# Kernel optimization log

Hardware: AMD Instinct MI355X
Metric: run time of the kernel (lower is better)

Reference implementation:

```python
import jax, jax.numpy as jnp
import numpy as np

B, S, D, H, DK, CR = 4, 4096, 1024, 16, 64, 3


def setup_inputs() -> dict:
    rng = jax.random.key(0)
    ks = jax.random.split(rng, 13)
    sc = 1.0 / np.sqrt(D)
    u = lambda k, shape: jax.random.uniform(k, shape, jnp.float32, -sc, sc)
    return {
        "query": jax.random.normal(ks[0], (B, S, D), jnp.float32),
        "key": jax.random.normal(ks[1], (B, S, D), jnp.float32),
        "value": jax.random.normal(ks[2], (B, S, D), jnp.float32),
        "Wq": u(ks[3], (D, D)), "bq": u(ks[4], (D,)),
        "Wk": u(ks[5], (D, D)), "bk": u(ks[6], (D,)),
        "Wv": u(ks[7], (D, D)), "bv": u(ks[8], (D,)),
        "Wo": u(ks[9], (D, D)), "bo": u(ks[10], (D,)),
        "conv_w": u(ks[11], (D, D, CR)),  # Conv1d(D, D, kernel=CR, stride=CR)
        "conv_b": u(ks[12], (D,)),
    }


def _compress(x, w, b):
    # x: (B, L, D) -> strided conv over L -> (B, ceil-ish L/CR, D)
    y = jax.lax.conv_general_dilated(
        x.transpose(0, 2, 1), w, window_strides=(CR,), padding="VALID",
        dimension_numbers=("NCH", "OIH", "NCH"))
    return (y + b[None, :, None]).transpose(0, 2, 1)


def reference(query, key, value, Wq, bq, Wk, bk, Wv, bv, Wo, bo, conv_w, conv_b):
    # Source quirk: pad amount derived from d_model (last dim), applied to seq.
    pad = CR - D % CR  # = 2 here
    if pad < CR:
        key = jnp.pad(key, ((0, 0), (pad, 0), (0, 0)))
        value = jnp.pad(value, ((0, 0), (pad, 0), (0, 0)))
    key = _compress(key, conv_w, conv_b)
    value = _compress(value, conv_w, conv_b)

    def proj(x, W, bias):  # (B, L, D) -> (B, H, L, DK)
        return (x @ W.T + bias).reshape(x.shape[0], -1, H, DK).transpose(0, 2, 1, 3)

    q = proj(query, Wq, bq)
    k = proj(key, Wk, bk)
    v = proj(value, Wv, bv)

    scores = jnp.einsum("bhqd,bhkd->bhqk", q, k) / np.float32(np.sqrt(DK))
    attn = jax.nn.softmax(scores, axis=-1)  # dropout is identity at eval
    x = jnp.einsum("bhqk,bhkd->bhqd", attn, v)
    x = x.transpose(0, 2, 1, 3).reshape(query.shape[0], -1, H * DK)
    return x @ Wo.T + bo
```

## Files before the change

### kernel.cpp

```cpp
#include <hip/hip_runtime.h>


#define DM   1024
#define NH   16
#define DKH  64
#define BB   4
#define SQ   4096
#define LCC  1366
#define LCP  1408
#define SPAD 4098
#define PSS  72

#define QSC  0.18033688011f

typedef unsigned short u16;
using short8 = __attribute__((ext_vector_type(8))) short;
using f32x4  = __attribute__((ext_vector_type(4))) float;
using us4    = __attribute__((ext_vector_type(4))) unsigned short;
using us8    = __attribute__((ext_vector_type(8))) unsigned short;

__device__ __forceinline__ u16 f2bf(float f) {
    unsigned u = __float_as_uint(f);
    u += 0x7fffu + ((u >> 16) & 1u);
    return (u16)(u >> 16);
}

__device__ __forceinline__ void gl_lds16(const void* g, void* l) {
    __builtin_amdgcn_global_load_lds(
        (__attribute__((address_space(1))) unsigned int*)(uintptr_t)g,
        (__attribute__((address_space(3))) unsigned int*)l,
        16, 0, 0);
}

__global__ __launch_bounds__(256) void cast4_k(const float* __restrict__ in, u16* __restrict__ out,
                                               int n4, float scale) {
    int i = blockIdx.x * 256 + threadIdx.x;
    if (i >= n4) return;
    float4 v = ((const float4*)in)[i];
    us4 o;
    o[0] = f2bf(v.x * scale); o[1] = f2bf(v.y * scale);
    o[2] = f2bf(v.z * scale); o[3] = f2bf(v.w * scale);
    ((us4*)out)[i] = o;
}

__global__ __launch_bounds__(256) void cast_pad_k(const float* __restrict__ in, u16* __restrict__ out) {
    int i = blockIdx.x * 256 + threadIdx.x;
    const int n4 = BB * SPAD * DM / 4;
    if (i >= n4) return;
    int e   = i * 4;
    int b   = e / (SPAD * DM);
    int rem = e - b * (SPAD * DM);
    int s   = rem >> 10;
    int d   = rem & (DM - 1);
    us4 o = {0, 0, 0, 0};
    if (s >= 2) {
        float4 v = *(const float4*)(in + (size_t)(b * SQ + (s - 2)) * DM + d);
        o[0] = f2bf(v.x); o[1] = f2bf(v.y); o[2] = f2bf(v.z); o[3] = f2bf(v.w);
    }
    ((us4*)out)[i] = o;
}

__global__ __launch_bounds__(256) void permcast_conv_k(const float* __restrict__ cw, u16* __restrict__ wc2) {
    int i = blockIdx.x * 256 + threadIdx.x;
    const int n4 = DM * DM * 3 / 4;
    if (i >= n4) return;
    int e   = i * 4;
    int o   = e / 3072;
    int rem = e - o * 3072;
    int r   = rem >> 10;
    int ii  = rem & 1023;
    us4 q;
    #pragma unroll
    for (int t = 0; t < 4; ++t) q[t] = f2bf(cw[(size_t)(o * DM + ii + t) * 3 + r]);
    ((us4*)wc2)[i] = q;
}

__global__ __launch_bounds__(256) void transpose_v_k(const u16* __restrict__ vp, u16* __restrict__ vt) {
    __shared__ u16 t[64 * 65];
    const int tid = threadIdx.x;
    const int j0 = blockIdx.x * 64;
    const int bh = blockIdx.y, b = bh >> 4, h = bh & 15;
    #pragma unroll
    for (int it = 0; it < 2; ++it) {
        int cc = tid + it * 256;
        int j = cc >> 3, d0 = (cc & 7) * 8;
        int jj = j0 + j;
        us8 v = {0, 0, 0, 0, 0, 0, 0, 0};
        if (jj < LCC) v = *(const us8*)(vp + (size_t)(b * LCC + jj) * DM + h * DKH + d0);
        #pragma unroll
        for (int q = 0; q < 8; ++q) t[(d0 + q) * 65 + j] = v[q];
    }
    __syncthreads();
    #pragma unroll
    for (int it = 0; it < 2; ++it) {
        int cc = tid + it * 256;
        int d = cc >> 3, q0 = (cc & 7) * 8;
        us8 v;
        #pragma unroll
        for (int q = 0; q < 8; ++q) {
            int cp = q0 + q;
            int k  = (cp & 3) * 16 + (cp >> 2);
            v[q] = t[d * 65 + k];
        }
        *(us8*)(vt + (size_t)(bh * DKH + d) * LCP + j0 + q0) = v;
    }
}

__global__ __launch_bounds__(256, 3) void gemm_mfma_k(
    const u16* __restrict__ A, const u16* __restrict__ Bw, const float* __restrict__ bias,
    void* __restrict__ C, int N, int K, int cf32, float bscale)
{
    __shared__ u16 As[128 * 64];
    __shared__ u16 Bs[128 * 64];
    const int tid = threadIdx.x, wave = tid >> 6, lane = tid & 63;
    const int quad = lane >> 4, l15 = lane & 15;
    const int n0 = blockIdx.y * 128, o0 = blockIdx.x * 128;
    const int wm = (wave >> 1) * 64, wn = (wave & 1) * 64;

    f32x4 acc[4][4];
    #pragma unroll
    for (int a = 0; a < 4; ++a)
        #pragma unroll
        for (int b = 0; b < 4; ++b)
            #pragma unroll
            for (int r = 0; r < 4; ++r) acc[a][b][r] = 0.0f;

    const int srow = (lane >> 3);
    const int sc8  = (lane & 7);

    for (int kt = 0; kt < K; kt += 64) {
        #pragma unroll
        for (int i = 0; i < 4; ++i) {
            int is  = wave * 4 + i;
            int row = is * 8 + srow;
            int c   = sc8 ^ (row & 7);
            int ra  = n0 + row; if (ra > N - 1) ra = N - 1;
            gl_lds16(A  + (size_t)ra * K + kt + c * 8,          As + is * 512 + lane * 8);
            gl_lds16(Bw + (size_t)(o0 + row) * K + kt + c * 8,  Bs + is * 512 + lane * 8);
        }
        __syncthreads();
        #pragma unroll
        for (int ks = 0; ks < 2; ++ks) {
            short8 af[4], bf[4];
            #pragma unroll
            for (int mi = 0; mi < 4; ++mi) {
                int m = wm + mi * 16 + l15;
                int c = (ks * 4 + quad) ^ (m & 7);
                af[mi] = *(const short8*)(As + m * 64 + c * 8);
            }
            #pragma unroll
            for (int nj = 0; nj < 4; ++nj) {
                int n = wn + nj * 16 + l15;
                int c = (ks * 4 + quad) ^ (n & 7);
                bf[nj] = *(const short8*)(Bs + n * 64 + c * 8);
            }
            #pragma unroll
            for (int mi = 0; mi < 4; ++mi)
                #pragma unroll
                for (int nj = 0; nj < 4; ++nj)
                    acc[mi][nj] = __builtin_amdgcn_mfma_f32_16x16x32_bf16(af[mi], bf[nj], acc[mi][nj], 0, 0, 0);
        }
        __syncthreads();
    }
    #pragma unroll
    for (int mi = 0; mi < 4; ++mi) {
        #pragma unroll
        for (int r = 0; r < 4; ++r) {
            int n = n0 + wm + mi * 16 + quad * 4 + r;
            if (n < N) {
                #pragma unroll
                for (int nj = 0; nj < 4; ++nj) {
                    int o = o0 + wn + nj * 16 + l15;
                    float v = acc[mi][nj][r] + bias[o] * bscale;
                    if (cf32) ((float*)C)[(size_t)n * DM + o] = v;
                    else      ((u16*)C)[(size_t)n * DM + o] = f2bf(v);
                }
            }
        }
    }
}

__global__ __launch_bounds__(256, 3) void attn_mfma_k(
    const u16* __restrict__ qp, const u16* __restrict__ kp,
    const u16* __restrict__ vt, u16* __restrict__ xo)
{
    __shared__ u16 Qs[128 * 64];
    __shared__ u16 Ks[64 * 64];
    __shared__ u16 Vts[64 * 64];
    __shared__ u16 Ps[128 * PSS];
    const int tid = threadIdx.x, wave = tid >> 6, lane = tid & 63;
    const int quad = lane >> 4, l15 = lane & 15;
    const int bh = blockIdx.y, b = bh >> 4, h = bh & 15;
    const int s0 = blockIdx.x * 128;
    const int wm = wave * 32;
    const int srow = (lane >> 3), sc8 = (lane & 7);

    #pragma unroll
    for (int i = 0; i < 4; ++i) {
        int is = wave * 4 + i;
        int row = is * 8 + srow;
        int c = sc8 ^ (row & 7);
        gl_lds16(qp + (size_t)(b * SQ + s0 + row) * DM + h * DKH + c * 8, Qs + is * 512 + lane * 8);
    }

    f32x4 oacc[2][4];
    #pragma unroll
    for (int a = 0; a < 2; ++a)
        #pragma unroll
        for (int d = 0; d < 4; ++d)
            #pragma unroll
            for (int r = 0; r < 4; ++r) oacc[a][d][r] = 0.0f;
    float lsum[2][4] = {{0.f, 0.f, 0.f, 0.f}, {0.f, 0.f, 0.f, 0.f}};

    for (int j0 = 0; j0 < LCC; j0 += 64) {
        #pragma unroll
        for (int i = 0; i < 2; ++i) {
            int is = wave * 2 + i;
            int row = is * 8 + srow;
            int c = sc8 ^ (row & 7);
            int j = j0 + row; if (j > LCC - 1) j = LCC - 1;
            gl_lds16(kp + (size_t)(b * LCC + j) * DM + h * DKH + c * 8, Ks + is * 512 + lane * 8);
            gl_lds16(vt + (size_t)(bh * DKH + row) * LCP + j0 + c * 8,  Vts + is * 512 + lane * 8);
        }
        __syncthreads();

        f32x4 sc[2][4];
        #pragma unroll
        for (int a = 0; a < 2; ++a)
            #pragma unroll
            for (int n = 0; n < 4; ++n)
                #pragma unroll
                for (int r = 0; r < 4; ++r) sc[a][n][r] = 0.0f;
        #pragma unroll
        for (int ks = 0; ks < 2; ++ks) {
            short8 aq[2], bk[4];
            #pragma unroll
            for (int mi = 0; mi < 2; ++mi) {
                int m = wm + mi * 16 + l15;
                int c = (ks * 4 + quad) ^ (m & 7);
                aq[mi] = *(const short8*)(Qs + m * 64 + c * 8);
            }
            #pragma unroll
            for (int nj = 0; nj < 4; ++nj) {
                int n = nj * 16 + l15;
                int c = (ks * 4 + quad) ^ (n & 7);
                bk[nj] = *(const short8*)(Ks + n * 64 + c * 8);
            }
            #pragma unroll
            for (int mi = 0; mi < 2; ++mi)
                #pragma unroll
                for (int nj = 0; nj < 4; ++nj)
                    sc[mi][nj] = __builtin_amdgcn_mfma_f32_16x16x32_bf16(aq[mi], bk[nj], sc[mi][nj], 0, 0, 0);
        }
        if (j0 + 64 > LCC) {
            #pragma unroll
            for (int nj = 0; nj < 4; ++nj) {
                if (j0 + nj * 16 + l15 >= LCC) {
                    #pragma unroll
                    for (int mi = 0; mi < 2; ++mi)
                        #pragma unroll
                        for (int r = 0; r < 4; ++r) sc[mi][nj][r] = -1e30f;
                }
            }
        }
        #pragma unroll
        for (int mi = 0; mi < 2; ++mi) {
            int pmb = wm + mi * 16 + quad * 4;
            #pragma unroll
            for (int r = 0; r < 4; ++r) {
                float p0 = __builtin_amdgcn_exp2f(sc[mi][0][r]);
                float p1 = __builtin_amdgcn_exp2f(sc[mi][1][r]);
                float p2 = __builtin_amdgcn_exp2f(sc[mi][2][r]);
                float p3 = __builtin_amdgcn_exp2f(sc[mi][3][r]);
                lsum[mi][r] += (p0 + p1) + (p2 + p3);
                unsigned w0, w1;
                asm("v_cvt_pk_bf16_f32 %0, %1, %2" : "=v"(w0) : "v"(p0), "v"(p1));
                asm("v_cvt_pk_bf16_f32 %0, %1, %2" : "=v"(w1) : "v"(p2), "v"(p3));
                uint2 pk; pk.x = w0; pk.y = w1;
                *(uint2*)(Ps + (pmb + r) * PSS + l15 * 4) = pk;
            }
        }
        #pragma unroll
        for (int ks = 0; ks < 2; ++ks) {
            short8 ap[2], bv[4];
            #pragma unroll
            for (int mi = 0; mi < 2; ++mi) {
                int m = wm + mi * 16 + l15;
                ap[mi] = *(const short8*)(Ps + m * PSS + ks * 32 + quad * 8);
            }
            #pragma unroll
            for (int dj = 0; dj < 4; ++dj) {
                int d = dj * 16 + l15;
                int c = (ks * 4 + quad) ^ (d & 7);
                bv[dj] = *(const short8*)(Vts + d * 64 + c * 8);
            }
            #pragma unroll
            for (int mi = 0; mi < 2; ++mi)
                #pragma unroll
                for (int dj = 0; dj < 4; ++dj)
                    oacc[mi][dj] = __builtin_amdgcn_mfma_f32_16x16x32_bf16(ap[mi], bv[dj], oacc[mi][dj], 0, 0, 0);
        }
        __syncthreads();
    }
    #pragma unroll
    for (int mi = 0; mi < 2; ++mi) {
        #pragma unroll
        for (int r = 0; r < 4; ++r) {
            float v = lsum[mi][r];
            v += __shfl_xor(v, 1, 64); v += __shfl_xor(v, 2, 64);
            v += __shfl_xor(v, 4, 64); v += __shfl_xor(v, 8, 64);
            float inv = 1.0f / v;
            int s = s0 + wm + mi * 16 + quad * 4 + r;
            #pragma unroll
            for (int dj = 0; dj < 4; ++dj)
                xo[(size_t)(b * SQ + s) * DM + h * DKH + dj * 16 + l15] = f2bf(oacc[mi][dj][r] * inv);
        }
    }
}

extern "C" void kernel_launch(void* const* d_in, const int* in_sizes, int n_in,
                              void* d_out, int out_size, void* d_ws, size_t ws_size,
                              hipStream_t stream)
{
    const float* query  = (const float*)d_in[0];
    const float* key    = (const float*)d_in[1];
    const float* value  = (const float*)d_in[2];
    const float* Wq     = (const float*)d_in[3];
    const float* bq     = (const float*)d_in[4];
    const float* Wk     = (const float*)d_in[5];
    const float* bk     = (const float*)d_in[6];
    const float* Wv     = (const float*)d_in[7];
    const float* bv     = (const float*)d_in[8];
    const float* Wo     = (const float*)d_in[9];
    const float* bo     = (const float*)d_in[10];
    const float* conv_w = (const float*)d_in[11];
    const float* conv_b = (const float*)d_in[12];
    float* out = (float*)d_out;

    u16* p = (u16*)d_ws;
    auto alloc = [&](size_t n) { u16* r = p; p += (n + 127) & ~(size_t)127; return r; };
    u16* qbf  = alloc((size_t)BB * SQ * DM);
    u16* kpad = alloc((size_t)BB * SPAD * DM);
    u16* vpad = alloc((size_t)BB * SPAD * DM);
    u16* wqb  = alloc((size_t)DM * DM);
    u16* wkb  = alloc((size_t)DM * DM);
    u16* wvb  = alloc((size_t)DM * DM);
    u16* wob  = alloc((size_t)DM * DM);
    u16* wc2b = alloc((size_t)DM * DM * 3);
    u16* kc   = alloc((size_t)BB * LCC * DM);
    u16* vc   = alloc((size_t)BB * LCC * DM);
    u16* kpj  = alloc((size_t)BB * LCC * DM);
    u16* vpj  = alloc((size_t)BB * LCC * DM);
    u16* qprj = alloc((size_t)BB * SQ * DM);
    u16* vtb  = alloc((size_t)BB * NH * DKH * LCP);
    u16* xo   = alloc((size_t)BB * SQ * DM);

    const int NC = BB * LCC;
    const int NS = BB * SQ;

    cast4_k<<<dim3(NS * DM / 4 / 256), 256, 0, stream>>>(query, qbf, NS * DM / 4, 1.0f);
    cast_pad_k<<<dim3((BB * SPAD * DM / 4 + 255) / 256), 256, 0, stream>>>(key, kpad);
    cast_pad_k<<<dim3((BB * SPAD * DM / 4 + 255) / 256), 256, 0, stream>>>(value, vpad);
    cast4_k<<<dim3(DM * DM / 4 / 256), 256, 0, stream>>>(Wq, wqb, DM * DM / 4, QSC);
    cast4_k<<<dim3(DM * DM / 4 / 256), 256, 0, stream>>>(Wk, wkb, DM * DM / 4, 1.0f);
    cast4_k<<<dim3(DM * DM / 4 / 256), 256, 0, stream>>>(Wv, wvb, DM * DM / 4, 1.0f);
    cast4_k<<<dim3(DM * DM / 4 / 256), 256, 0, stream>>>(Wo, wob, DM * DM / 4, 1.0f);
    permcast_conv_k<<<dim3(DM * DM * 3 / 4 / 256), 256, 0, stream>>>(conv_w, wc2b);

    gemm_mfma_k<<<dim3(8, 43), 256, 0, stream>>>(kpad, wc2b, conv_b, kc, NC, 3072, 0, 1.0f);
    gemm_mfma_k<<<dim3(8, 43), 256, 0, stream>>>(vpad, wc2b, conv_b, vc, NC, 3072, 0, 1.0f);

    gemm_mfma_k<<<dim3(8, 128), 256, 0, stream>>>(qbf, wqb, bq, qprj, NS, DM, 0, QSC);
    gemm_mfma_k<<<dim3(8, 43), 256, 0, stream>>>(kc, wkb, bk, kpj, NC, DM, 0, 1.0f);
    gemm_mfma_k<<<dim3(8, 43), 256, 0, stream>>>(vc, wvb, bv, vpj, NC, DM, 0, 1.0f);

    transpose_v_k<<<dim3(22, BB * NH), 256, 0, stream>>>(vpj, vtb);

    attn_mfma_k<<<dim3(SQ / 128, BB * NH), 256, 0, stream>>>(qprj, kpj, vtb, xo);

    gemm_mfma_k<<<dim3(8, 128), 256, 0, stream>>>(xo, wob, bo, out, NS, DM, 1, 1.0f);
}
```

Baseline: 670.5 us.

## Double-buffer K/V in attention, keep P in registers, batch paired launches

```diff
diff --git a/kernel.cpp b/kernel.cpp
--- a/kernel.cpp
+++ b/kernel.cpp
@@ -9,7 +9,6 @@
 #define LCC  1366
 #define LCP  1408
 #define SPAD 4098
-#define PSS  72
 
 #define QSC  0.18033688011f
 
@@ -43,7 +42,10 @@
     ((us4*)out)[i] = o;
 }
 
-__global__ __launch_bounds__(256) void cast_pad_k(const float* __restrict__ in, u16* __restrict__ out) {
+__global__ __launch_bounds__(256) void cast_pad2_k(const float* __restrict__ in0, u16* __restrict__ out0,
+                                                   const float* __restrict__ in1, u16* __restrict__ out1) {
+    const float* in = blockIdx.z ? in1 : in0;
+    u16* out        = blockIdx.z ? out1 : out0;
     int i = blockIdx.x * 256 + threadIdx.x;
     const int n4 = BB * SPAD * DM / 4;
     if (i >= n4) return;
@@ -99,7 +101,8 @@
         #pragma unroll
         for (int q = 0; q < 8; ++q) {
             int cp = q0 + q;
-            int k  = (cp & 3) * 16 + (cp >> 2);
+            int ks = cp >> 5, qd = (cp >> 3) & 3, j = cp & 7;
+            int k  = (ks + 2 * (j >> 2)) * 16 + qd * 4 + (j & 3);
             v[q] = t[d * 65 + k];
         }
         *(us8*)(vt + (size_t)(bh * DKH + d) * LCP + j0 + q0) = v;
@@ -107,9 +110,15 @@
 }
 
 __global__ __launch_bounds__(256, 3) void gemm_mfma_k(
-    const u16* __restrict__ A, const u16* __restrict__ Bw, const float* __restrict__ bias,
-    void* __restrict__ C, int N, int K, int cf32, float bscale)
+    const u16* __restrict__ A0, const u16* __restrict__ B0, const float* __restrict__ bias0, void* __restrict__ C0,
+    const u16* __restrict__ A1, const u16* __restrict__ B1, const float* __restrict__ bias1, void* __restrict__ C1,
+    int N, int K, int cf32, float bscale)
 {
+    const u16* A     = blockIdx.z ? A1 : A0;
+    const u16* Bw    = blockIdx.z ? B1 : B0;
+    const float* bias = blockIdx.z ? bias1 : bias0;
+    void* C          = blockIdx.z ? C1 : C0;
+
     __shared__ u16 As[128 * 64];
     __shared__ u16 Bs[128 * 64];
     const int tid = threadIdx.x, wave = tid >> 6, lane = tid & 63;
@@ -184,24 +193,34 @@
     const u16* __restrict__ qp, const u16* __restrict__ kp,
     const u16* __restrict__ vt, u16* __restrict__ xo)
 {
-    __shared__ u16 Qs[128 * 64];
-    __shared__ u16 Ks[64 * 64];
-    __shared__ u16 Vts[64 * 64];
-    __shared__ u16 Ps[128 * PSS];
+    __shared__ u16 lds[4 * 4096];
     const int tid = threadIdx.x, wave = tid >> 6, lane = tid & 63;
     const int quad = lane >> 4, l15 = lane & 15;
     const int bh = blockIdx.y, b = bh >> 4, h = bh & 15;
     const int s0 = blockIdx.x * 128;
-    const int wm = wave * 32;
-    const int srow = (lane >> 3), sc8 = (lane & 7);
+    const int wq = wave * 32;
+    const int srow = lane >> 3, sc8 = lane & 7;
 
     #pragma unroll
     for (int i = 0; i < 4; ++i) {
         int is = wave * 4 + i;
         int row = is * 8 + srow;
         int c = sc8 ^ (row & 7);
-        gl_lds16(qp + (size_t)(b * SQ + s0 + row) * DM + h * DKH + c * 8, Qs + is * 512 + lane * 8);
-    }
+        gl_lds16(qp + (size_t)(b * SQ + s0 + row) * DM + h * DKH + c * 8,
+                 lds + is * 512 + lane * 8);
+    }
+    __syncthreads();
+    short8 qfr[2][2];
+    #pragma unroll
+    for (int qg = 0; qg < 2; ++qg) {
+        int m = wq + qg * 16 + l15;
+        #pragma unroll
+        for (int ks = 0; ks < 2; ++ks) {
+            int c = (ks * 4 + quad) ^ (m & 7);
+            qfr[qg][ks] = *(const short8*)(lds + m * 64 + c * 8);
+        }
+    }
+    __syncthreads();
 
     f32x4 oacc[2][4];
     #pragma unroll
@@ -210,19 +229,37 @@
         for (int d = 0; d < 4; ++d)
             #pragma unroll
             for (int r = 0; r < 4; ++r) oacc[a][d][r] = 0.0f;
-    float lsum[2][4] = {{0.f, 0.f, 0.f, 0.f}, {0.f, 0.f, 0.f, 0.f}};
-
-    for (int j0 = 0; j0 < LCC; j0 += 64) {
-        #pragma unroll
-        for (int i = 0; i < 2; ++i) {
-            int is = wave * 2 + i;
-            int row = is * 8 + srow;
-            int c = sc8 ^ (row & 7);
-            int j = j0 + row; if (j > LCC - 1) j = LCC - 1;
-            gl_lds16(kp + (size_t)(b * LCC + j) * DM + h * DKH + c * 8, Ks + is * 512 + lane * 8);
-            gl_lds16(vt + (size_t)(bh * DKH + row) * LCP + j0 + c * 8,  Vts + is * 512 + lane * 8);
-        }
+    float lsum[2] = {0.f, 0.f};
+
+    #pragma unroll
+    for (int i = 0; i < 2; ++i) {
+        int is = wave * 2 + i;
+        int row = is * 8 + srow;
+        int c = sc8 ^ (row & 7);
+        int j = row; if (j > LCC - 1) j = LCC - 1;
+        gl_lds16(kp + (size_t)(b * LCC + j) * DM + h * DKH + c * 8, lds + is * 512 + lane * 8);
+        gl_lds16(vt + (size_t)(bh * DKH + row) * LCP + c * 8,       lds + 4096 + is * 512 + lane * 8);
+    }
+
+    int cur = 0;
+    for (int t = 0; t < 22; ++t) {
+        const int j0 = t * 64;
         __syncthreads();
+        if (t < 21) {
+            int nj0 = j0 + 64;
+            u16* base = lds + (cur ^ 1) * 8192;
+            #pragma unroll
+            for (int i = 0; i < 2; ++i) {
+                int is = wave * 2 + i;
+                int row = is * 8 + srow;
+                int c = sc8 ^ (row & 7);
+                int j = nj0 + row; if (j > LCC - 1) j = LCC - 1;
+                gl_lds16(kp + (size_t)(b * LCC + j) * DM + h * DKH + c * 8, base + is * 512 + lane * 8);
+                gl_lds16(vt + (size_t)(bh * DKH + row) * LCP + nj0 + c * 8, base + 4096 + is * 512 + lane * 8);
+            }
+        }
+        const u16* Kb = lds + cur * 8192;
+        const u16* Vb = Kb + 4096;
 
         f32x4 sc[2][4];
         #pragma unroll
@@ -231,89 +268,90 @@
             for (int n = 0; n < 4; ++n)
                 #pragma unroll
                 for (int r = 0; r < 4; ++r) sc[a][n][r] = 0.0f;
+        __builtin_amdgcn_s_setprio(1);
         #pragma unroll
         for (int ks = 0; ks < 2; ++ks) {
-            short8 aq[2], bk[4];
-            #pragma unroll
-            for (int mi = 0; mi < 2; ++mi) {
-                int m = wm + mi * 16 + l15;
-                int c = (ks * 4 + quad) ^ (m & 7);
-                aq[mi] = *(const short8*)(Qs + m * 64 + c * 8);
-            }
+            short8 kfr[4];
             #pragma unroll
             for (int nj = 0; nj < 4; ++nj) {
                 int n = nj * 16 + l15;
                 int c = (ks * 4 + quad) ^ (n & 7);
-                bk[nj] = *(const short8*)(Ks + n * 64 + c * 8);
-            }
-            #pragma unroll
-            for (int mi = 0; mi < 2; ++mi)
+                kfr[nj] = *(const short8*)(Kb + n * 64 + c * 8);
+            }
+            #pragma unroll
+            for (int qg = 0; qg < 2; ++qg)
                 #pragma unroll
                 for (int nj = 0; nj < 4; ++nj)
-                    sc[mi][nj] = __builtin_amdgcn_mfma_f32_16x16x32_bf16(aq[mi], bk[nj], sc[mi][nj], 0, 0, 0);
-        }
-        if (j0 + 64 > LCC) {
+                    sc[qg][nj] = __builtin_amdgcn_mfma_f32_16x16x32_bf16(kfr[nj], qfr[qg][ks], sc[qg][nj], 0, 0, 0);
+        }
+        __builtin_amdgcn_s_setprio(0);
+
+        const bool tail = (j0 + 64 > LCC);
+        #pragma unroll
+        for (int qg = 0; qg < 2; ++qg) {
             #pragma unroll
             for (int nj = 0; nj < 4; ++nj) {
-                if (j0 + nj * 16 + l15 >= LCC) {
-                    #pragma unroll
-                    for (int mi = 0; mi < 2; ++mi)
-                        #pragma unroll
-                        for (int r = 0; r < 4; ++r) sc[mi][nj][r] = -1e30f;
+                #pragma unroll
+                for (int r = 0; r < 4; ++r) {
+                    float p = __builtin_amdgcn_exp2f(sc[qg][nj][r]);
+                    if (tail && (j0 + nj * 16 + quad * 4 + r) >= LCC) p = 0.0f;
+                    sc[qg][nj][r] = p;
+                    lsum[qg] += p;
                 }
             }
         }
-        #pragma unroll
-        for (int mi = 0; mi < 2; ++mi) {
-            int pmb = wm + mi * 16 + quad * 4;
-            #pragma unroll
-            for (int r = 0; r < 4; ++r) {
-                float p0 = __builtin_amdgcn_exp2f(sc[mi][0][r]);
-                float p1 = __builtin_amdgcn_exp2f(sc[mi][1][r]);
-                float p2 = __builtin_amdgcn_exp2f(sc[mi][2][r]);
-                float p3 = __builtin_amdgcn_exp2f(sc[mi][3][r]);
-                lsum[mi][r] += (p0 + p1) + (p2 + p3);
-                unsigned w0, w1;
-                asm("v_cvt_pk_bf16_f32 %0, %1, %2" : "=v"(w0) : "v"(p0), "v"(p1));
-                asm("v_cvt_pk_bf16_f32 %0, %1, %2" : "=v"(w1) : "v"(p2), "v"(p3));
-                uint2 pk; pk.x = w0; pk.y = w1;
-                *(uint2*)(Ps + (pmb + r) * PSS + l15 * 4) = pk;
-            }
-        }
+        short8 pa[2][2];
+        #pragma unroll
+        for (int qg = 0; qg < 2; ++qg) {
+            #pragma unroll
+            for (int ks = 0; ks < 2; ++ks) {
+                unsigned w0, w1, w2, w3;
+                asm("v_cvt_pk_bf16_f32 %0, %1, %2" : "=v"(w0) : "v"(sc[qg][ks][0]),     "v"(sc[qg][ks][1]));
+                asm("v_cvt_pk_bf16_f32 %0, %1, %2" : "=v"(w1) : "v"(sc[qg][ks][2]),     "v"(sc[qg][ks][3]));
+                asm("v_cvt_pk_bf16_f32 %0, %1, %2" : "=v"(w2) : "v"(sc[qg][ks + 2][0]), "v"(sc[qg][ks + 2][1]));
+                asm("v_cvt_pk_bf16_f32 %0, %1, %2" : "=v"(w3) : "v"(sc[qg][ks + 2][2]), "v"(sc[qg][ks + 2][3]));
+                union { unsigned u[4]; short8 s; } cv;
+                cv.u[0] = w0; cv.u[1] = w1; cv.u[2] = w2; cv.u[3] = w3;
+                pa[qg][ks] = cv.s;
+            }
+        }
+        __builtin_amdgcn_s_setprio(1);
         #pragma unroll
         for (int ks = 0; ks < 2; ++ks) {
-            short8 ap[2], bv[4];
-            #pragma unroll
-            for (int mi = 0; mi < 2; ++mi) {
-                int m = wm + mi * 16 + l15;
-                ap[mi] = *(const short8*)(Ps + m * PSS + ks * 32 + quad * 8);
-            }
+            short8 vfr[4];
             #pragma unroll
             for (int dj = 0; dj < 4; ++dj) {
                 int d = dj * 16 + l15;
                 int c = (ks * 4 + quad) ^ (d & 7);
-                bv[dj] = *(const short8*)(Vts + d * 64 + c * 8);
-            }
-            #pragma unroll
-            for (int mi = 0; mi < 2; ++mi)
+                vfr[dj] = *(const short8*)(Vb + d * 64 + c * 8);
+            }
+            #pragma unroll
+            for (int qg = 0; qg < 2; ++qg)
                 #pragma unroll
                 for (int dj = 0; dj < 4; ++dj)
-                    oacc[mi][dj] = __builtin_amdgcn_mfma_f32_16x16x32_bf16(ap[mi], bv[dj], oacc[mi][dj], 0, 0, 0);
-        }
-        __syncthreads();
-    }
-    #pragma unroll
-    for (int mi = 0; mi < 2; ++mi) {
+                    oacc[qg][dj] = __builtin_amdgcn_mfma_f32_16x16x32_bf16(pa[qg][ks], vfr[dj], oacc[qg][dj], 0, 0, 0);
+        }
+        __builtin_amdgcn_s_setprio(0);
+        cur ^= 1;
+    }
+
+    #pragma unroll
+    for (int qg = 0; qg < 2; ++qg) {
+        float v = lsum[qg];
+        v += __shfl_xor(v, 16, 64);
+        v += __shfl_xor(v, 32, 64);
+        lsum[qg] = v;
+    }
+    #pragma unroll
+    for (int qg = 0; qg < 2; ++qg) {
         #pragma unroll
         for (int r = 0; r < 4; ++r) {
-            float v = lsum[mi][r];
-            v += __shfl_xor(v, 1, 64); v += __shfl_xor(v, 2, 64);
-            v += __shfl_xor(v, 4, 64); v += __shfl_xor(v, 8, 64);
-            float inv = 1.0f / v;
-            int s = s0 + wm + mi * 16 + quad * 4 + r;
+            float tot = __shfl(lsum[qg], quad * 4 + r, 64);
+            float inv = 1.0f / tot;
+            int s = s0 + wq + qg * 16 + quad * 4 + r;
             #pragma unroll
             for (int dj = 0; dj < 4; ++dj)
-                xo[(size_t)(b * SQ + s) * DM + h * DKH + dj * 16 + l15] = f2bf(oacc[mi][dj][r] * inv);
+                xo[(size_t)(b * SQ + s) * DM + h * DKH + dj * 16 + l15] = f2bf(oacc[qg][dj][r] * inv);
         }
     }
 }
@@ -359,24 +397,25 @@
     const int NS = BB * SQ;
 
     cast4_k<<<dim3(NS * DM / 4 / 256), 256, 0, stream>>>(query, qbf, NS * DM / 4, 1.0f);
-    cast_pad_k<<<dim3((BB * SPAD * DM / 4 + 255) / 256), 256, 0, stream>>>(key, kpad);
-    cast_pad_k<<<dim3((BB * SPAD * DM / 4 + 255) / 256), 256, 0, stream>>>(value, vpad);
+    cast_pad2_k<<<dim3((BB * SPAD * DM / 4 + 255) / 256, 1, 2), 256, 0, stream>>>(key, kpad, value, vpad);
     cast4_k<<<dim3(DM * DM / 4 / 256), 256, 0, stream>>>(Wq, wqb, DM * DM / 4, QSC);
     cast4_k<<<dim3(DM * DM / 4 / 256), 256, 0, stream>>>(Wk, wkb, DM * DM / 4, 1.0f);
     cast4_k<<<dim3(DM * DM / 4 / 256), 256, 0, stream>>>(Wv, wvb, DM * DM / 4, 1.0f);
     cast4_k<<<dim3(DM * DM / 4 / 256), 256, 0, stream>>>(Wo, wob, DM * DM / 4, 1.0f);
     permcast_conv_k<<<dim3(DM * DM * 3 / 4 / 256), 256, 0, stream>>>(conv_w, wc2b);
 
-    gemm_mfma_k<<<dim3(8, 43), 256, 0, stream>>>(kpad, wc2b, conv_b, kc, NC, 3072, 0, 1.0f);
-    gemm_mfma_k<<<dim3(8, 43), 256, 0, stream>>>(vpad, wc2b, conv_b, vc, NC, 3072, 0, 1.0f);
-
-    gemm_mfma_k<<<dim3(8, 128), 256, 0, stream>>>(qbf, wqb, bq, qprj, NS, DM, 0, QSC);
-    gemm_mfma_k<<<dim3(8, 43), 256, 0, stream>>>(kc, wkb, bk, kpj, NC, DM, 0, 1.0f);
-    gemm_mfma_k<<<dim3(8, 43), 256, 0, stream>>>(vc, wvb, bv, vpj, NC, DM, 0, 1.0f);
+    gemm_mfma_k<<<dim3(8, 43, 2), 256, 0, stream>>>(kpad, wc2b, conv_b, kc,
+                                                    vpad, wc2b, conv_b, vc, NC, 3072, 0, 1.0f);
+
+    gemm_mfma_k<<<dim3(8, 128, 1), 256, 0, stream>>>(qbf, wqb, bq, qprj,
+                                                     qbf, wqb, bq, qprj, NS, DM, 0, QSC);
+    gemm_mfma_k<<<dim3(8, 43, 2), 256, 0, stream>>>(kc, wkb, bk, kpj,
+                                                    vc, wvb, bv, vpj, NC, DM, 0, 1.0f);
 
     transpose_v_k<<<dim3(22, BB * NH), 256, 0, stream>>>(vpj, vtb);
 
     attn_mfma_k<<<dim3(SQ / 128, BB * NH), 256, 0, stream>>>(qprj, kpj, vtb, xo);
 
-    gemm_mfma_k<<<dim3(8, 128), 256, 0, stream>>>(xo, wob, bo, out, NS, DM, 1, 1.0f);
-}
+    gemm_mfma_k<<<dim3(8, 128, 1), 256, 0, stream>>>(xo, wob, bo, out,
+                                                     xo, wob, bo, out, NS, DM, 1, 1.0f);
+}
```

New measurement: 603.2 us. -10.0%, faster.
